# Performance work log

Measured on AMD Instinct MI355X. Metric: run time of the kernel, lower is better.

The kernel has to match this reference:

```python
import jax, jax.numpy as jnp
import numpy as np

N, K, G = 4096, 4096, 128  # out_features, in_features, groupsize


def setup_inputs() -> dict:
    key = jax.random.key(0)
    k1, k2, k3, k4 = jax.random.split(key, 4)
    input = jax.random.normal(k1, (1, 2048, K), dtype=jnp.float32)
    # packed int4 weights: each byte holds two 4-bit codes (high nibble = even k, low = odd k)
    weight_packed = jax.random.randint(k2, (N, K // 2), 0, 256, dtype=jnp.int32)
    scales = jax.random.uniform(k3, (K // G, N), dtype=jnp.float32) * 0.02 + 1e-3
    zeros = jax.random.normal(k4, (K // G, N), dtype=jnp.float32) * 0.05
    scales_and_zeros = jnp.stack([scales, zeros], axis=-1)  # (K//G, N, 2)
    return {"input": input, "weight_packed": weight_packed,
            "scales_and_zeros": scales_and_zeros, "groupsize": G}


def reference(input, weight_packed, scales_and_zeros, groupsize):
    n, k_half = weight_packed.shape
    k = 2 * k_half
    g = k // groupsize
    # unpack two int4 codes per byte: high nibble first (even k index), then low nibble
    hi = (weight_packed >> 4) & 0xF
    lo = weight_packed & 0xF
    q = jnp.stack([hi, lo], axis=-1).reshape(n, k)  # (N, K), codes in [0,15]
    scales = scales_and_zeros[..., 0].T  # (N, G)
    zeros = scales_and_zeros[..., 1].T   # (N, G)
    # group-wise affine dequant: w = (q - 8) * scale + zero
    qg = q.reshape(n, g, groupsize).astype(jnp.float32)
    w = (qg - 8.0) * scales[:, :, None] + zeros[:, :, None]  # (N, G, gs)
    w = w.reshape(n, k)
    # out[..., n] = sum_k input[..., k] * w[n, k]
    return jnp.einsum('bsk,nk->bsn', input, w)
```

## Files before the change

### kernel.cpp

```cpp
#include <hip/hip_runtime.h>
#include <hip/hip_bf16.h>


using bf16x8 = __attribute__((ext_vector_type(8))) short;
using f32x16 = __attribute__((ext_vector_type(16))) float;

#define KK 4096
#define NN 4096
#define NT (KK / 64)

static __device__ __forceinline__ short f2bf(float f) {
    __hip_bfloat16 h = __float2bfloat16(f);
    return __builtin_bit_cast(short, h);
}

#define GLDS16(gptr, lptr) __builtin_amdgcn_global_load_lds( \
    (const __attribute__((address_space(1))) void*)(gptr),   \
    (__attribute__((address_space(3))) void*)(lptr), 16, 0, 0)

#define MFMA32 __builtin_amdgcn_mfma_f32_32x32x16_bf16

__global__ __launch_bounds__(256) void dequant_w(
    const int* __restrict__ W, const float* __restrict__ SZ,
    short* __restrict__ Wd)
{
    const int idx = blockIdx.x * 256 + threadIdx.x;
    const int n   = idx >> 9;
    const int q4  = idx & 511;
    const int kh0 = q4 << 2;
    const int g   = kh0 >> 6;
    const float2 sz = *(const float2*)(SZ + ((size_t)g * NN + n) * 2);
    const float scale = sz.x;
    const float zs    = sz.y - 8.0f * sz.x;
    int4 p = *(const int4*)(W + (size_t)n * (KK / 2) + kh0);
    int vals[4] = {p.x, p.y, p.z, p.w};
    bf16x8 r;
    #pragma unroll
    for (int j = 0; j < 4; ++j) {
        int v = vals[j];
        r[2 * j]     = f2bf((float)((v >> 4) & 0xF) * scale + zs);
        r[2 * j + 1] = f2bf((float)(v & 0xF) * scale + zs);
    }
    *(bf16x8*)&Wd[(size_t)n * KK + (kh0 << 1)] = r;
}

__global__ __launch_bounds__(256) void cvt_a(
    const float* __restrict__ A, short* __restrict__ Ab)
{
    const int idx = blockIdx.x * 256 + threadIdx.x;
    const float4* s = (const float4*)(A + (size_t)idx * 8);
    float4 u = s[0], v = s[1];
    bf16x8 r;
    r[0] = f2bf(u.x); r[1] = f2bf(u.y); r[2] = f2bf(u.z); r[3] = f2bf(u.w);
    r[4] = f2bf(v.x); r[5] = f2bf(v.y); r[6] = f2bf(v.z); r[7] = f2bf(v.w);
    *(bf16x8*)&Ab[(size_t)idx * 8] = r;
}

__global__ __launch_bounds__(512, 2) void gemm_pl(
    const short* __restrict__ Ab, const short* __restrict__ Bb,
    float* __restrict__ C)
{
    __shared__ short sA[3 * 256 * 64];
    __shared__ short sB[3 * 128 * 64];

    const int tid  = threadIdx.x;
    const int lane = tid & 63;
    const int wave = tid >> 6;
    const int wm   = wave >> 1;
    const int wn   = wave & 1;
    const int bm   = blockIdx.y * 256;
    const int bn   = blockIdx.x * 128;

    const int sl = lane >> 3;
    const int sc = (lane & 7) ^ sl;
    const short* aSt = Ab + (size_t)(bm + wave * 32 + sl) * KK + sc * 8;
    const short* bSt = Bb + (size_t)(bn + wave * 16 + sl) * KK + sc * 8;

    const int l31 = lane & 31;
    const int lx  = lane >> 5;
    const int l7  = lane & 7;
    const int px0 = ((0 + lx) ^ l7) * 8;
    const int px1 = ((2 + lx) ^ l7) * 8;
    const int px2 = ((4 + lx) ^ l7) * 8;
    const int px3 = ((6 + lx) ^ l7) * 8;
    const int aRd = (wm * 64 + l31) * 64;
    const int bRd = (wn * 64 + l31) * 64;

    f32x16 acc00 = {}, acc01 = {}, acc10 = {}, acc11 = {};
    bf16x8 pA00, pA01, pA10, pA11, pB00, pB01, pB10, pB11;
    bf16x8 qA00, qA01, qA10, qA11, qB00, qB01, qB10, qB11;

    #pragma unroll
    for (int l = 0; l < 4; ++l)
        GLDS16(aSt + (size_t)l * 8 * KK,      &sA[(wave * 32 + l * 8) * 64]);
    #pragma unroll
    for (int l = 0; l < 2; ++l)
        GLDS16(bSt + (size_t)l * 8 * KK,      &sB[(wave * 16 + l * 8) * 64]);
    #pragma unroll
    for (int l = 0; l < 4; ++l)
        GLDS16(aSt + (size_t)l * 8 * KK + 64, &sA[16384 + (wave * 32 + l * 8) * 64]);
    #pragma unroll
    for (int l = 0; l < 2; ++l)
        GLDS16(bSt + (size_t)l * 8 * KK + 64, &sB[8192 + (wave * 16 + l * 8) * 64]);
    asm volatile("s_waitcnt vmcnt(6)" ::: "memory");
    __builtin_amdgcn_s_barrier();

    pA00 = *(const bf16x8*)&sA[aRd + px0];
    pA01 = *(const bf16x8*)&sA[aRd + px1];
    pA10 = *(const bf16x8*)&sA[aRd + 2048 + px0];
    pA11 = *(const bf16x8*)&sA[aRd + 2048 + px1];
    pB00 = *(const bf16x8*)&sB[bRd + px0];
    pB01 = *(const bf16x8*)&sB[bRd + px1];
    pB10 = *(const bf16x8*)&sB[bRd + 2048 + px0];
    pB11 = *(const bf16x8*)&sB[bRd + 2048 + px1];
    asm volatile("s_waitcnt lgkmcnt(0)" ::: "memory");
    __builtin_amdgcn_sched_barrier(0);

    int cur = 0;
    for (int t = 0; t < NT; ++t) {
        const int nxt1 = (cur == 2) ? 0 : cur + 1;
        const int nxt2 = (nxt1 == 2) ? 0 : nxt1 + 1;
        const short* sAc = &sA[cur * 16384];
        const short* sBc = &sB[cur * 8192];
        const short* sA1 = &sA[nxt1 * 16384];
        const short* sB1 = &sB[nxt1 * 8192];
        short* sAn = &sA[nxt2 * 16384];
        short* sBn = &sB[nxt2 * 8192];
        const bool st = (t + 2 < NT);
        const int gk = (t + 2) * 64;

        qA00 = *(const bf16x8*)&sAc[aRd + px2];
        qA01 = *(const bf16x8*)&sAc[aRd + px3];
        qA10 = *(const bf16x8*)&sAc[aRd + 2048 + px2];
        qA11 = *(const bf16x8*)&sAc[aRd + 2048 + px3];
        qB00 = *(const bf16x8*)&sBc[bRd + px2];
        qB01 = *(const bf16x8*)&sBc[bRd + px3];
        qB10 = *(const bf16x8*)&sBc[bRd + 2048 + px2];
        qB11 = *(const bf16x8*)&sBc[bRd + 2048 + px3];
        if (st) {
            GLDS16(aSt + (size_t)0 * 8 * KK + gk, sAn + (wave * 32 + 0) * 64);
            GLDS16(aSt + (size_t)1 * 8 * KK + gk, sAn + (wave * 32 + 8) * 64);
            GLDS16(bSt + (size_t)0 * 8 * KK + gk, sBn + (wave * 16 + 0) * 64);
        }
        __builtin_amdgcn_sched_barrier(0);

        __builtin_amdgcn_s_setprio(1);
        acc00 = MFMA32(pA00, pB00, acc00, 0, 0, 0);
        acc00 = MFMA32(pA01, pB01, acc00, 0, 0, 0);
        acc01 = MFMA32(pA00, pB10, acc01, 0, 0, 0);
        acc01 = MFMA32(pA01, pB11, acc01, 0, 0, 0);
        acc10 = MFMA32(pA10, pB00, acc10, 0, 0, 0);
        acc10 = MFMA32(pA11, pB01, acc10, 0, 0, 0);
        acc11 = MFMA32(pA10, pB10, acc11, 0, 0, 0);
        acc11 = MFMA32(pA11, pB11, acc11, 0, 0, 0);
        __builtin_amdgcn_s_setprio(0);

        asm volatile("s_waitcnt lgkmcnt(0)" ::: "memory");
        __builtin_amdgcn_sched_barrier(0);
        if (t < NT - 2) {
            asm volatile("s_waitcnt vmcnt(3)" ::: "memory");
        } else {
            asm volatile("s_waitcnt vmcnt(0)" ::: "memory");
        }
        __builtin_amdgcn_s_barrier();

        if (t + 1 < NT) {
            pA00 = *(const bf16x8*)&sA1[aRd + px0];
            pA01 = *(const bf16x8*)&sA1[aRd + px1];
            pA10 = *(const bf16x8*)&sA1[aRd + 2048 + px0];
            pA11 = *(const bf16x8*)&sA1[aRd + 2048 + px1];
            pB00 = *(const bf16x8*)&sB1[bRd + px0];
            pB01 = *(const bf16x8*)&sB1[bRd + px1];
            pB10 = *(const bf16x8*)&sB1[bRd + 2048 + px0];
            pB11 = *(const bf16x8*)&sB1[bRd + 2048 + px1];
        }
        if (st) {
            GLDS16(aSt + (size_t)2 * 8 * KK + gk, sAn + (wave * 32 + 16) * 64);
            GLDS16(aSt + (size_t)3 * 8 * KK + gk, sAn + (wave * 32 + 24) * 64);
            GLDS16(bSt + (size_t)1 * 8 * KK + gk, sBn + (wave * 16 + 8) * 64);
        }
        __builtin_amdgcn_sched_barrier(0);

        __builtin_amdgcn_s_setprio(1);
        acc00 = MFMA32(qA00, qB00, acc00, 0, 0, 0);
        acc00 = MFMA32(qA01, qB01, acc00, 0, 0, 0);
        acc01 = MFMA32(qA00, qB10, acc01, 0, 0, 0);
        acc01 = MFMA32(qA01, qB11, acc01, 0, 0, 0);
        acc10 = MFMA32(qA10, qB00, acc10, 0, 0, 0);
        acc10 = MFMA32(qA11, qB01, acc10, 0, 0, 0);
        acc11 = MFMA32(qA10, qB10, acc11, 0, 0, 0);
        acc11 = MFMA32(qA11, qB11, acc11, 0, 0, 0);
        __builtin_amdgcn_s_setprio(0);

        asm volatile("s_waitcnt lgkmcnt(0)" ::: "memory");
        __builtin_amdgcn_sched_barrier(0);

        cur = nxt1;
    }

    {
        const int crow = lx * 4;
        float* Cp = C + (size_t)(bm + wm * 64) * NN + bn + wn * 64;
        #pragma unroll
        for (int m = 0; m < 2; ++m) {
            #pragma unroll
            for (int qr = 0; qr < 4; ++qr) {
                #pragma unroll
                for (int j = 0; j < 4; ++j) {
                    const int row = m * 32 + crow + j + 8 * qr;
                    float* dst = Cp + (size_t)row * NN + l31;
                    if (m == 0) {
                        dst[0]  = acc00[qr * 4 + j];
                        dst[32] = acc01[qr * 4 + j];
                    } else {
                        dst[0]  = acc10[qr * 4 + j];
                        dst[32] = acc11[qr * 4 + j];
                    }
                }
            }
        }
    }
}

using f32x4 = __attribute__((ext_vector_type(4))) float;
#define LDKF 72
__global__ __launch_bounds__(256) void wq4_gemm_fused(
    const float* __restrict__ A, const int* __restrict__ W,
    const float* __restrict__ SZ, float* __restrict__ C, int M)
{
    __shared__ short sA[128 * LDKF];
    __shared__ short sB[128 * LDKF];
    const int tid = threadIdx.x, lane = tid & 63, wave = tid >> 6;
    const int wr = (wave >> 1) << 6, wc = (wave & 1) << 6;
    const int bm = blockIdx.y * 128, bn = blockIdx.x * 128;
    const int ar = tid >> 2, ac = (tid & 3) << 4;
    const int br = tid >> 1, bh = (tid & 1) << 4;
    const float* Arow0 = A + (size_t)(bm + ar) * KK + ac;
    const float* Arow1 = A + (size_t)(bm + 64 + ar) * KK + ac;
    const int*   Wrow  = W + (size_t)(bn + br) * (KK / 2) + bh;
    const float* SZrow = SZ + (size_t)(bn + br) * 2;
    f32x4 acc[4][4] = {};
    for (int k0 = 0; k0 < KK; k0 += 64) {
        {
            const float4* s0 = (const float4*)(Arow0 + k0);
            const float4* s1 = (const float4*)(Arow1 + k0);
            float4 a0 = s0[0], a1 = s0[1], a2 = s0[2], a3 = s0[3];
            float4 b0 = s1[0], b1 = s1[1], b2 = s1[2], b3 = s1[3];
            auto cvt8 = [](float4 u, float4 v) -> bf16x8 {
                bf16x8 r;
                r[0] = f2bf(u.x); r[1] = f2bf(u.y); r[2] = f2bf(u.z); r[3] = f2bf(u.w);
                r[4] = f2bf(v.x); r[5] = f2bf(v.y); r[6] = f2bf(v.z); r[7] = f2bf(v.w);
                return r;
            };
            *(bf16x8*)&sA[ar * LDKF + ac]            = cvt8(a0, a1);
            *(bf16x8*)&sA[ar * LDKF + ac + 8]        = cvt8(a2, a3);
            *(bf16x8*)&sA[(64 + ar) * LDKF + ac]     = cvt8(b0, b1);
            *(bf16x8*)&sA[(64 + ar) * LDKF + ac + 8] = cvt8(b2, b3);
        }
        {
            const int g = k0 >> 7;
            const float2 sz = *(const float2*)(SZrow + (size_t)g * NN * 2);
            const float scale = sz.x, zs = sz.y - 8.0f * sz.x;
            const int4* src = (const int4*)(Wrow + (k0 >> 1));
            #pragma unroll
            for (int i = 0; i < 4; ++i) {
                int4 p = src[i];
                int vals[4] = {p.x, p.y, p.z, p.w};
                bf16x8 r;
                #pragma unroll
                for (int j = 0; j < 4; ++j) {
                    int v = vals[j];
                    r[2 * j]     = f2bf((float)((v >> 4) & 0xF) * scale + zs);
                    r[2 * j + 1] = f2bf((float)(v & 0xF) * scale + zs);
                }
                *(bf16x8*)&sB[br * LDKF + (bh << 1) + (i << 3)] = r;
            }
        }
        __syncthreads();
        #pragma unroll
        for (int ks = 0; ks < 2; ++ks) {
            const int col = (ks << 5) + ((lane >> 4) << 3);
            bf16x8 af[4], bfr[4];
            #pragma unroll
            for (int m = 0; m < 4; ++m)
                af[m] = *(const bf16x8*)&sA[(wr + m * 16 + (lane & 15)) * LDKF + col];
            #pragma unroll
            for (int n = 0; n < 4; ++n)
                bfr[n] = *(const bf16x8*)&sB[(wc + n * 16 + (lane & 15)) * LDKF + col];
            #pragma unroll
            for (int m = 0; m < 4; ++m)
                #pragma unroll
                for (int n = 0; n < 4; ++n)
                    acc[m][n] = __builtin_amdgcn_mfma_f32_16x16x32_bf16(
                        af[m], bfr[n], acc[m][n], 0, 0, 0);
        }
        __syncthreads();
    }
    float* Cp = C + (size_t)(bm + wr) * NN + bn + wc;
    const int cr = (lane >> 4) << 2, cc = lane & 15;
    #pragma unroll
    for (int m = 0; m < 4; ++m)
        #pragma unroll
        for (int j = 0; j < 4; ++j) {
            float* dst = Cp + (size_t)(m * 16 + cr + j) * NN + cc;
            #pragma unroll
            for (int n = 0; n < 4; ++n) dst[n * 16] = acc[m][n][j];
        }
}

extern "C" void kernel_launch(void* const* d_in, const int* in_sizes, int n_in,
                              void* d_out, int out_size, void* d_ws, size_t ws_size,
                              hipStream_t stream) {
    const float* A  = (const float*)d_in[0];
    const int*   W  = (const int*)d_in[1];
    const float* SZ = (const float*)d_in[2];
    float* C = (float*)d_out;

    const int M = in_sizes[0] / KK;

    const size_t wd_elems = (size_t)NN * KK;
    const size_t ab_elems = (size_t)M * KK;
    const size_t need = (wd_elems + ab_elems) * sizeof(short);

    if (ws_size >= need && (M % 256) == 0) {
        short* Wd = (short*)d_ws;
        short* Ab = Wd + wd_elems;
        dequant_w<<<NN * (KK / 8) / 256, 256, 0, stream>>>(W, SZ, Wd);
        cvt_a<<<(int)(ab_elems / 8 / 256), 256, 0, stream>>>(A, Ab);
        dim3 grid(NN / 128, M / 256);
        gemm_pl<<<grid, dim3(512), 0, stream>>>(Ab, Wd, C);
    } else {
        dim3 grid(NN / 128, M / 128);
        wq4_gemm_fused<<<grid, dim3(256), 0, stream>>>(A, W, SZ, C, M);
    }
}
```

Baseline: 93.78 us.

## Interleave LDS fragment loads with MFMA at finer k-slice granularity

Splits each 64-wide k tile into four 16-wide slices and double-buffers register fragments (even/odd sets) so each slice's LDS reads are issued while the previous slice's MFMAs run. This halves the fragment register footprint and removes the explicit lgkmcnt(0) waits between MFMA groups, relying on compiler-inserted waits. It adds more scheduling barriers and smaller MFMA batches, which could expose LDS latency if the compiler's waits are placed poorly.

```diff
diff --git a/kernel.cpp b/kernel.cpp
--- a/kernel.cpp
+++ b/kernel.cpp
@@ -19,6 +19,7 @@
     (__attribute__((address_space(3))) void*)(lptr), 16, 0, 0)
 
 #define MFMA32 __builtin_amdgcn_mfma_f32_32x32x16_bf16
+#define SBAR() __builtin_amdgcn_sched_barrier(0)
 
 __global__ __launch_bounds__(256) void dequant_w(
     const int* __restrict__ W, const float* __restrict__ SZ,
@@ -87,8 +88,8 @@
     const int bRd = (wn * 64 + l31) * 64;
 
     f32x16 acc00 = {}, acc01 = {}, acc10 = {}, acc11 = {};
-    bf16x8 pA00, pA01, pA10, pA11, pB00, pB01, pB10, pB11;
-    bf16x8 qA00, qA01, qA10, qA11, qB00, qB01, qB10, qB11;
+    bf16x8 eA0, eA1, eB0, eB1;
+    bf16x8 oA0, oA1, oB0, oB1;
 
     #pragma unroll
     for (int l = 0; l < 4; ++l)
@@ -105,16 +106,11 @@
     asm volatile("s_waitcnt vmcnt(6)" ::: "memory");
     __builtin_amdgcn_s_barrier();
 
-    pA00 = *(const bf16x8*)&sA[aRd + px0];
-    pA01 = *(const bf16x8*)&sA[aRd + px1];
-    pA10 = *(const bf16x8*)&sA[aRd + 2048 + px0];
-    pA11 = *(const bf16x8*)&sA[aRd + 2048 + px1];
-    pB00 = *(const bf16x8*)&sB[bRd + px0];
-    pB01 = *(const bf16x8*)&sB[bRd + px1];
-    pB10 = *(const bf16x8*)&sB[bRd + 2048 + px0];
-    pB11 = *(const bf16x8*)&sB[bRd + 2048 + px1];
-    asm volatile("s_waitcnt lgkmcnt(0)" ::: "memory");
-    __builtin_amdgcn_sched_barrier(0);
+    eA0 = *(const bf16x8*)&sA[aRd + px0];
+    eA1 = *(const bf16x8*)&sA[aRd + 2048 + px0];
+    eB0 = *(const bf16x8*)&sB[bRd + px0];
+    eB1 = *(const bf16x8*)&sB[bRd + 2048 + px0];
+    SBAR();
 
     int cur = 0;
     for (int t = 0; t < NT; ++t) {
@@ -129,34 +125,52 @@
         const bool st = (t + 2 < NT);
         const int gk = (t + 2) * 64;
 
-        qA00 = *(const bf16x8*)&sAc[aRd + px2];
-        qA01 = *(const bf16x8*)&sAc[aRd + px3];
-        qA10 = *(const bf16x8*)&sAc[aRd + 2048 + px2];
-        qA11 = *(const bf16x8*)&sAc[aRd + 2048 + px3];
-        qB00 = *(const bf16x8*)&sBc[bRd + px2];
-        qB01 = *(const bf16x8*)&sBc[bRd + px3];
-        qB10 = *(const bf16x8*)&sBc[bRd + 2048 + px2];
-        qB11 = *(const bf16x8*)&sBc[bRd + 2048 + px3];
+        oA0 = *(const bf16x8*)&sAc[aRd + px1];
+        oA1 = *(const bf16x8*)&sAc[aRd + 2048 + px1];
+        oB0 = *(const bf16x8*)&sBc[bRd + px1];
+        oB1 = *(const bf16x8*)&sBc[bRd + 2048 + px1];
+        SBAR();
+        __builtin_amdgcn_s_setprio(1);
+        acc00 = MFMA32(eA0, eB0, acc00, 0, 0, 0);
+        acc01 = MFMA32(eA0, eB1, acc01, 0, 0, 0);
+        acc10 = MFMA32(eA1, eB0, acc10, 0, 0, 0);
+        acc11 = MFMA32(eA1, eB1, acc11, 0, 0, 0);
+        __builtin_amdgcn_s_setprio(0);
+        SBAR();
+
+        eA0 = *(const bf16x8*)&sAc[aRd + px2];
+        eA1 = *(const bf16x8*)&sAc[aRd + 2048 + px2];
+        eB0 = *(const bf16x8*)&sBc[bRd + px2];
+        eB1 = *(const bf16x8*)&sBc[bRd + 2048 + px2];
+        SBAR();
+        __builtin_amdgcn_s_setprio(1);
+        acc00 = MFMA32(oA0, oB0, acc00, 0, 0, 0);
+        acc01 = MFMA32(oA0, oB1, acc01, 0, 0, 0);
+        acc10 = MFMA32(oA1, oB0, acc10, 0, 0, 0);
+        acc11 = MFMA32(oA1, oB1, acc11, 0, 0, 0);
+        __builtin_amdgcn_s_setprio(0);
+        SBAR();
+
+        oA0 = *(const bf16x8*)&sAc[aRd + px3];
+        oA1 = *(const bf16x8*)&sAc[aRd + 2048 + px3];
+        oB0 = *(const bf16x8*)&sBc[bRd + px3];
+        oB1 = *(const bf16x8*)&sBc[bRd + 2048 + px3];
         if (st) {
             GLDS16(aSt + (size_t)0 * 8 * KK + gk, sAn + (wave * 32 + 0) * 64);
             GLDS16(aSt + (size_t)1 * 8 * KK + gk, sAn + (wave * 32 + 8) * 64);
             GLDS16(bSt + (size_t)0 * 8 * KK + gk, sBn + (wave * 16 + 0) * 64);
         }
-        __builtin_amdgcn_sched_barrier(0);
-
+        SBAR();
         __builtin_amdgcn_s_setprio(1);
-        acc00 = MFMA32(pA00, pB00, acc00, 0, 0, 0);
-        acc00 = MFMA32(pA01, pB01, acc00, 0, 0, 0);
-        acc01 = MFMA32(pA00, pB10, acc01, 0, 0, 0);
-        acc01 = MFMA32(pA01, pB11, acc01, 0, 0, 0);
-        acc10 = MFMA32(pA10, pB00, acc10, 0, 0, 0);
-        acc10 = MFMA32(pA11, pB01, acc10, 0, 0, 0);
-        acc11 = MFMA32(pA10, pB10, acc11, 0, 0, 0);
-        acc11 = MFMA32(pA11, pB11, acc11, 0, 0, 0);
+        acc00 = MFMA32(eA0, eB0, acc00, 0, 0, 0);
+        acc01 = MFMA32(eA0, eB1, acc01, 0, 0, 0);
+        acc10 = MFMA32(eA1, eB0, acc10, 0, 0, 0);
+        acc11 = MFMA32(eA1, eB1, acc11, 0, 0, 0);
         __builtin_amdgcn_s_setprio(0);
+        SBAR();
 
         asm volatile("s_waitcnt lgkmcnt(0)" ::: "memory");
-        __builtin_amdgcn_sched_barrier(0);
+        SBAR();
         if (t < NT - 2) {
             asm volatile("s_waitcnt vmcnt(3)" ::: "memory");
         } else {
@@ -165,35 +179,24 @@
         __builtin_amdgcn_s_barrier();
 
         if (t + 1 < NT) {
-            pA00 = *(const bf16x8*)&sA1[aRd + px0];
-            pA01 = *(const bf16x8*)&sA1[aRd + px1];
-            pA10 = *(const bf16x8*)&sA1[aRd + 2048 + px0];
-            pA11 = *(const bf16x8*)&sA1[aRd + 2048 + px1];
-            pB00 = *(const bf16x8*)&sB1[bRd + px0];
-            pB01 = *(const bf16x8*)&sB1[bRd + px1];
-            pB10 = *(const bf16x8*)&sB1[bRd + 2048 + px0];
-            pB11 = *(const bf16x8*)&sB1[bRd + 2048 + px1];
+            eA0 = *(const bf16x8*)&sA1[aRd + px0];
+            eA1 = *(const bf16x8*)&sA1[aRd + 2048 + px0];
+            eB0 = *(const bf16x8*)&sB1[bRd + px0];
+            eB1 = *(const bf16x8*)&sB1[bRd + 2048 + px0];
         }
         if (st) {
             GLDS16(aSt + (size_t)2 * 8 * KK + gk, sAn + (wave * 32 + 16) * 64);
             GLDS16(aSt + (size_t)3 * 8 * KK + gk, sAn + (wave * 32 + 24) * 64);
             GLDS16(bSt + (size_t)1 * 8 * KK + gk, sBn + (wave * 16 + 8) * 64);
         }
-        __builtin_amdgcn_sched_barrier(0);
-
+        SBAR();
         __builtin_amdgcn_s_setprio(1);
-        acc00 = MFMA32(qA00, qB00, acc00, 0, 0, 0);
-        acc00 = MFMA32(qA01, qB01, acc00, 0, 0, 0);
-        acc01 = MFMA32(qA00, qB10, acc01, 0, 0, 0);
-        acc01 = MFMA32(qA01, qB11, acc01, 0, 0, 0);
-        acc10 = MFMA32(qA10, qB00, acc10, 0, 0, 0);
-        acc10 = MFMA32(qA11, qB01, acc10, 0, 0, 0);
-        acc11 = MFMA32(qA10, qB10, acc11, 0, 0, 0);
-        acc11 = MFMA32(qA11, qB11, acc11, 0, 0, 0);
+        acc00 = MFMA32(oA0, oB0, acc00, 0, 0, 0);
+        acc01 = MFMA32(oA0, oB1, acc01, 0, 0, 0);
+        acc10 = MFMA32(oA1, oB0, acc10, 0, 0, 0);
+        acc11 = MFMA32(oA1, oB1, acc11, 0, 0, 0);
         __builtin_amdgcn_s_setprio(0);
-
-        asm volatile("s_waitcnt lgkmcnt(0)" ::: "memory");
-        __builtin_amdgcn_sched_barrier(0);
+        SBAR();
 
         cur = nxt1;
     }
```

Result: slower. 96.23 us (+2.6%).

## Fuse int4 weight dequantization into GEMM mainloop, dropping separate dequant pass

Applied to the files above, without the earlier changes.

Removes the standalone dequant kernel that wrote a full bf16 weight matrix to workspace. The GEMM now loads packed int4 weights and scale/zero pairs into registers, dequantizes them, and writes bf16 tiles to swizzled LDS inside the pipelined loop. All A tile loads move to the first half of each iteration. This removes a large global write and read round trip. In exchange it adds per-block redundant dequant ALU work, register pressure and LDS stores on the MFMA critical path.

```diff
diff --git a/kernel.cpp b/kernel.cpp
--- a/kernel.cpp
+++ b/kernel.cpp
@@ -19,29 +19,17 @@
     (__attribute__((address_space(3))) void*)(lptr), 16, 0, 0)
 
 #define MFMA32 __builtin_amdgcn_mfma_f32_32x32x16_bf16
-
-__global__ __launch_bounds__(256) void dequant_w(
-    const int* __restrict__ W, const float* __restrict__ SZ,
-    short* __restrict__ Wd)
-{
-    const int idx = blockIdx.x * 256 + threadIdx.x;
-    const int n   = idx >> 9;
-    const int q4  = idx & 511;
-    const int kh0 = q4 << 2;
-    const int g   = kh0 >> 6;
-    const float2 sz = *(const float2*)(SZ + ((size_t)g * NN + n) * 2);
-    const float scale = sz.x;
-    const float zs    = sz.y - 8.0f * sz.x;
-    int4 p = *(const int4*)(W + (size_t)n * (KK / 2) + kh0);
-    int vals[4] = {p.x, p.y, p.z, p.w};
+#define SBAR() __builtin_amdgcn_sched_barrier(0)
+
+static __device__ __forceinline__ bf16x8 dq8(int4 p, float s, float zs) {
     bf16x8 r;
+    int v[4] = {p.x, p.y, p.z, p.w};
     #pragma unroll
     for (int j = 0; j < 4; ++j) {
-        int v = vals[j];
-        r[2 * j]     = f2bf((float)((v >> 4) & 0xF) * scale + zs);
-        r[2 * j + 1] = f2bf((float)(v & 0xF) * scale + zs);
-    }
-    *(bf16x8*)&Wd[(size_t)n * KK + (kh0 << 1)] = r;
+        r[2 * j]     = f2bf((float)((v[j] >> 4) & 0xF) * s + zs);
+        r[2 * j + 1] = f2bf((float)(v[j] & 0xF) * s + zs);
+    }
+    return r;
 }
 
 __global__ __launch_bounds__(256) void cvt_a(
@@ -56,9 +44,9 @@
     *(bf16x8*)&Ab[(size_t)idx * 8] = r;
 }
 
-__global__ __launch_bounds__(512, 2) void gemm_pl(
-    const short* __restrict__ Ab, const short* __restrict__ Bb,
-    float* __restrict__ C)
+__global__ __launch_bounds__(512, 2) void gemm_fq(
+    const short* __restrict__ Ab, const int* __restrict__ W,
+    const float* __restrict__ SZ, float* __restrict__ C)
 {
     __shared__ short sA[3 * 256 * 64];
     __shared__ short sB[3 * 128 * 64];
@@ -74,7 +62,13 @@
     const int sl = lane >> 3;
     const int sc = (lane & 7) ^ sl;
     const short* aSt = Ab + (size_t)(bm + wave * 32 + sl) * KK + sc * 8;
-    const short* bSt = Bb + (size_t)(bn + wave * 16 + sl) * KK + sc * 8;
+
+    const int brow = wave * 16 + (lane >> 2);
+    const int bl4  = lane & 3;
+    const int* wSt = W + (size_t)(bn + brow) * (KK / 2) + bl4 * 8;
+    const float* szp = SZ + (size_t)(bn + brow) * 2;
+    const int bw0 = brow * 64 + (((bl4 * 2))     ^ (brow & 7)) * 8;
+    const int bw1 = brow * 64 + (((bl4 * 2) | 1) ^ (brow & 7)) * 8;
 
     const int l31 = lane & 31;
     const int lx  = lane >> 5;
@@ -90,19 +84,26 @@
     bf16x8 pA00, pA01, pA10, pA11, pB00, pB01, pB10, pB11;
     bf16x8 qA00, qA01, qA10, qA11, qB00, qB01, qB10, qB11;
 
+    int4 b00p = *(const int4*)(wSt + 0);
+    int4 b01p = *(const int4*)(wSt + 4);
+    float2 sz0 = *(const float2*)(szp);
+    int4 b10p = *(const int4*)(wSt + 32);
+    int4 b11p = *(const int4*)(wSt + 36);
     #pragma unroll
     for (int l = 0; l < 4; ++l)
         GLDS16(aSt + (size_t)l * 8 * KK,      &sA[(wave * 32 + l * 8) * 64]);
     #pragma unroll
-    for (int l = 0; l < 2; ++l)
-        GLDS16(bSt + (size_t)l * 8 * KK,      &sB[(wave * 16 + l * 8) * 64]);
-    #pragma unroll
     for (int l = 0; l < 4; ++l)
         GLDS16(aSt + (size_t)l * 8 * KK + 64, &sA[16384 + (wave * 32 + l * 8) * 64]);
-    #pragma unroll
-    for (int l = 0; l < 2; ++l)
-        GLDS16(bSt + (size_t)l * 8 * KK + 64, &sB[8192 + (wave * 16 + l * 8) * 64]);
-    asm volatile("s_waitcnt vmcnt(6)" ::: "memory");
+    {
+        const float s = sz0.x, zs = sz0.y - 8.0f * sz0.x;
+        *(bf16x8*)&sB[bw0]        = dq8(b00p, s, zs);
+        *(bf16x8*)&sB[bw1]        = dq8(b01p, s, zs);
+        *(bf16x8*)&sB[8192 + bw0] = dq8(b10p, s, zs);
+        *(bf16x8*)&sB[8192 + bw1] = dq8(b11p, s, zs);
+    }
+    asm volatile("s_waitcnt vmcnt(4)" ::: "memory");
+    asm volatile("s_waitcnt lgkmcnt(0)" ::: "memory");
     __builtin_amdgcn_s_barrier();
 
     pA00 = *(const bf16x8*)&sA[aRd + px0];
@@ -114,7 +115,7 @@
     pB10 = *(const bf16x8*)&sB[bRd + 2048 + px0];
     pB11 = *(const bf16x8*)&sB[bRd + 2048 + px1];
     asm volatile("s_waitcnt lgkmcnt(0)" ::: "memory");
-    __builtin_amdgcn_sched_barrier(0);
+    SBAR();
 
     int cur = 0;
     for (int t = 0; t < NT; ++t) {
@@ -137,12 +138,17 @@
         qB01 = *(const bf16x8*)&sBc[bRd + px3];
         qB10 = *(const bf16x8*)&sBc[bRd + 2048 + px2];
         qB11 = *(const bf16x8*)&sBc[bRd + 2048 + px3];
+        int4 bp0, bp1; float2 szv;
         if (st) {
+            bp0 = *(const int4*)(wSt + (gk >> 1));
+            bp1 = *(const int4*)(wSt + (gk >> 1) + 4);
+            szv = *(const float2*)(szp + (size_t)((t + 2) >> 1) * NN * 2);
             GLDS16(aSt + (size_t)0 * 8 * KK + gk, sAn + (wave * 32 + 0) * 64);
             GLDS16(aSt + (size_t)1 * 8 * KK + gk, sAn + (wave * 32 + 8) * 64);
-            GLDS16(bSt + (size_t)0 * 8 * KK + gk, sBn + (wave * 16 + 0) * 64);
-        }
-        __builtin_amdgcn_sched_barrier(0);
+            GLDS16(aSt + (size_t)2 * 8 * KK + gk, sAn + (wave * 32 + 16) * 64);
+            GLDS16(aSt + (size_t)3 * 8 * KK + gk, sAn + (wave * 32 + 24) * 64);
+        }
+        SBAR();
 
         __builtin_amdgcn_s_setprio(1);
         acc00 = MFMA32(pA00, pB00, acc00, 0, 0, 0);
@@ -155,13 +161,19 @@
         acc11 = MFMA32(pA11, pB11, acc11, 0, 0, 0);
         __builtin_amdgcn_s_setprio(0);
 
-        asm volatile("s_waitcnt lgkmcnt(0)" ::: "memory");
-        __builtin_amdgcn_sched_barrier(0);
-        if (t < NT - 2) {
-            asm volatile("s_waitcnt vmcnt(3)" ::: "memory");
+        if (st) {
+            asm volatile("s_waitcnt vmcnt(4)" ::: "memory");
         } else {
             asm volatile("s_waitcnt vmcnt(0)" ::: "memory");
         }
+        SBAR();
+        if (st) {
+            const float s = szv.x, zs = szv.y - 8.0f * szv.x;
+            *(bf16x8*)&sBn[bw0] = dq8(bp0, s, zs);
+            *(bf16x8*)&sBn[bw1] = dq8(bp1, s, zs);
+        }
+        asm volatile("s_waitcnt lgkmcnt(0)" ::: "memory");
+        SBAR();
         __builtin_amdgcn_s_barrier();
 
         if (t + 1 < NT) {
@@ -174,12 +186,7 @@
             pB10 = *(const bf16x8*)&sB1[bRd + 2048 + px0];
             pB11 = *(const bf16x8*)&sB1[bRd + 2048 + px1];
         }
-        if (st) {
-            GLDS16(aSt + (size_t)2 * 8 * KK + gk, sAn + (wave * 32 + 16) * 64);
-            GLDS16(aSt + (size_t)3 * 8 * KK + gk, sAn + (wave * 32 + 24) * 64);
-            GLDS16(bSt + (size_t)1 * 8 * KK + gk, sBn + (wave * 16 + 8) * 64);
-        }
-        __builtin_amdgcn_sched_barrier(0);
+        SBAR();
 
         __builtin_amdgcn_s_setprio(1);
         acc00 = MFMA32(qA00, qB00, acc00, 0, 0, 0);
@@ -193,7 +200,7 @@
         __builtin_amdgcn_s_setprio(0);
 
         asm volatile("s_waitcnt lgkmcnt(0)" ::: "memory");
-        __builtin_amdgcn_sched_barrier(0);
+        SBAR();
 
         cur = nxt1;
     }
@@ -318,17 +325,14 @@
 
     const int M = in_sizes[0] / KK;
 
-    const size_t wd_elems = (size_t)NN * KK;
     const size_t ab_elems = (size_t)M * KK;
-    const size_t need = (wd_elems + ab_elems) * sizeof(short);
+    const size_t need = ab_elems * sizeof(short);
 
     if (ws_size >= need && (M % 256) == 0) {
-        short* Wd = (short*)d_ws;
-        short* Ab = Wd + wd_elems;
-        dequant_w<<<NN * (KK / 8) / 256, 256, 0, stream>>>(W, SZ, Wd);
+        short* Ab = (short*)d_ws;
         cvt_a<<<(int)(ab_elems / 8 / 256), 256, 0, stream>>>(A, Ab);
         dim3 grid(NN / 128, M / 256);
-        gemm_pl<<<grid, dim3(512), 0, stream>>>(Ab, Wd, C);
+        gemm_fq<<<grid, dim3(512), 0, stream>>>(Ab, W, SZ, C);
     } else {
         dim3 grid(NN / 128, M / 128);
         wq4_gemm_fused<<<grid, dim3(256), 0, stream>>>(A, W, SZ, C, M);
```

Result: slower. 104.0 us (+10.9%).

## Add split-K 256x256-tile GEMM with bf16 partials and reduction kernel

Applied to the files above, without the earlier changes.

Adds a new GEMM path that splits K into two halves across blockIdx.z, using larger 256x256 output tiles per block with double-buffered LDS and eight accumulators per wave. Each half writes bf16 partial results to workspace, and a separate reduce kernel sums them into fp32 output. The aim is better grid occupancy and more MFMA reuse per loaded tile. In exchange it adds extra global traffic for the partials, one more launch, and precision loss from rounding partials to bf16. It also needs a larger workspace and falls back to the old path when that is unavailable.

```diff
diff --git a/kernel.cpp b/kernel.cpp
--- a/kernel.cpp
+++ b/kernel.cpp
@@ -4,21 +4,26 @@
 
 using bf16x8 = __attribute__((ext_vector_type(8))) short;
 using f32x16 = __attribute__((ext_vector_type(16))) float;
+using f32x4  = __attribute__((ext_vector_type(4))) float;
 
 #define KK 4096
 #define NN 4096
-#define NT (KK / 64)
 
 static __device__ __forceinline__ short f2bf(float f) {
     __hip_bfloat16 h = __float2bfloat16(f);
     return __builtin_bit_cast(short, h);
 }
+static __device__ __forceinline__ float bf2f(short u) {
+    unsigned x = ((unsigned)(unsigned short)u) << 16;
+    return __builtin_bit_cast(float, x);
+}
 
 #define GLDS16(gptr, lptr) __builtin_amdgcn_global_load_lds( \
     (const __attribute__((address_space(1))) void*)(gptr),   \
     (__attribute__((address_space(3))) void*)(lptr), 16, 0, 0)
 
 #define MFMA32 __builtin_amdgcn_mfma_f32_32x32x16_bf16
+#define SBAR() __builtin_amdgcn_sched_barrier(0)
 
 __global__ __launch_bounds__(256) void dequant_w(
     const int* __restrict__ W, const float* __restrict__ SZ,
@@ -56,25 +61,26 @@
     *(bf16x8*)&Ab[(size_t)idx * 8] = r;
 }
 
-__global__ __launch_bounds__(512, 2) void gemm_pl(
-    const short* __restrict__ Ab, const short* __restrict__ Bb,
-    float* __restrict__ C)
+__global__ __launch_bounds__(512, 2) void gemm_sk(
+    const short* __restrict__ Ab, const short* __restrict__ Wd,
+    unsigned short* __restrict__ P, int M)
 {
-    __shared__ short sA[3 * 256 * 64];
-    __shared__ short sB[3 * 128 * 64];
+    __shared__ short sA[2 * 256 * 64];
+    __shared__ short sB[2 * 256 * 64];
 
     const int tid  = threadIdx.x;
     const int lane = tid & 63;
     const int wave = tid >> 6;
-    const int wm   = wave >> 1;
-    const int wn   = wave & 1;
+    const int wm   = wave >> 2;
+    const int wn   = wave & 3;
     const int bm   = blockIdx.y * 256;
-    const int bn   = blockIdx.x * 128;
+    const int bn   = blockIdx.x * 256;
+    const size_t kz = (size_t)blockIdx.z * 2048;
 
     const int sl = lane >> 3;
     const int sc = (lane & 7) ^ sl;
-    const short* aSt = Ab + (size_t)(bm + wave * 32 + sl) * KK + sc * 8;
-    const short* bSt = Bb + (size_t)(bn + wave * 16 + sl) * KK + sc * 8;
+    const short* aSt = Ab + (size_t)(bm + wave * 32 + sl) * KK + kz + sc * 8;
+    const short* bSt = Wd + (size_t)(bn + wave * 32 + sl) * KK + kz + sc * 8;
 
     const int l31 = lane & 31;
     const int lx  = lane >> 5;
@@ -83,13 +89,173 @@
     const int px1 = ((2 + lx) ^ l7) * 8;
     const int px2 = ((4 + lx) ^ l7) * 8;
     const int px3 = ((6 + lx) ^ l7) * 8;
-    const int aRd = (wm * 64 + l31) * 64;
+    const int aRd = (wm * 128 + l31) * 64;
     const int bRd = (wn * 64 + l31) * 64;
 
+    f32x16 acc00 = {}, acc01 = {}, acc10 = {}, acc11 = {};
+    f32x16 acc20 = {}, acc21 = {}, acc30 = {}, acc31 = {};
+    bf16x8 eA0, eA1, eA2, eA3, eB0, eB1;
+    bf16x8 oA0, oA1, oA2, oA3, oB0, oB1;
+
+    #pragma unroll
+    for (int l = 0; l < 4; ++l)
+        GLDS16(aSt + (size_t)l * 8 * KK, &sA[(wave * 32 + l * 8) * 64]);
+    #pragma unroll
+    for (int l = 0; l < 4; ++l)
+        GLDS16(bSt + (size_t)l * 8 * KK, &sB[(wave * 32 + l * 8) * 64]);
+    asm volatile("s_waitcnt vmcnt(0)" ::: "memory");
+    __builtin_amdgcn_s_barrier();
+
+    eA0 = *(const bf16x8*)&sA[aRd + px0];
+    eA1 = *(const bf16x8*)&sA[aRd + 2048 + px0];
+    eA2 = *(const bf16x8*)&sA[aRd + 4096 + px0];
+    eA3 = *(const bf16x8*)&sA[aRd + 6144 + px0];
+    eB0 = *(const bf16x8*)&sB[bRd + px0];
+    eB1 = *(const bf16x8*)&sB[bRd + 2048 + px0];
+    asm volatile("s_waitcnt lgkmcnt(0)" ::: "memory");
+    SBAR();
+
+#define MM8(XA0, XA1, XA2, XA3, XB0, XB1)            \
+    __builtin_amdgcn_s_setprio(1);                   \
+    acc00 = MFMA32(XA0, XB0, acc00, 0, 0, 0);        \
+    acc01 = MFMA32(XA0, XB1, acc01, 0, 0, 0);        \
+    acc10 = MFMA32(XA1, XB0, acc10, 0, 0, 0);        \
+    acc11 = MFMA32(XA1, XB1, acc11, 0, 0, 0);        \
+    acc20 = MFMA32(XA2, XB0, acc20, 0, 0, 0);        \
+    acc21 = MFMA32(XA2, XB1, acc21, 0, 0, 0);        \
+    acc30 = MFMA32(XA3, XB0, acc30, 0, 0, 0);        \
+    acc31 = MFMA32(XA3, XB1, acc31, 0, 0, 0);        \
+    __builtin_amdgcn_s_setprio(0);
+
+    for (int t = 0; t < 32; ++t) {
+        const int cur = t & 1;
+        const short* sAc = &sA[cur * 16384];
+        const short* sBc = &sB[cur * 16384];
+        short* sAn = &sA[(cur ^ 1) * 16384];
+        short* sBn = &sB[(cur ^ 1) * 16384];
+        const bool st = (t + 1 < 32);
+        const size_t gk = (size_t)(t + 1) * 64;
+
+        oA0 = *(const bf16x8*)&sAc[aRd + px1];
+        oA1 = *(const bf16x8*)&sAc[aRd + 2048 + px1];
+        oA2 = *(const bf16x8*)&sAc[aRd + 4096 + px1];
+        oA3 = *(const bf16x8*)&sAc[aRd + 6144 + px1];
+        oB0 = *(const bf16x8*)&sBc[bRd + px1];
+        oB1 = *(const bf16x8*)&sBc[bRd + 2048 + px1];
+        if (st) {
+            GLDS16(aSt + (size_t)0 * 8 * KK + gk, sAn + (wave * 32 + 0) * 64);
+            GLDS16(aSt + (size_t)1 * 8 * KK + gk, sAn + (wave * 32 + 8) * 64);
+            GLDS16(aSt + (size_t)2 * 8 * KK + gk, sAn + (wave * 32 + 16) * 64);
+            GLDS16(aSt + (size_t)3 * 8 * KK + gk, sAn + (wave * 32 + 24) * 64);
+        }
+        SBAR();
+        MM8(eA0, eA1, eA2, eA3, eB0, eB1)
+        SBAR();
+
+        eA0 = *(const bf16x8*)&sAc[aRd + px2];
+        eA1 = *(const bf16x8*)&sAc[aRd + 2048 + px2];
+        eA2 = *(const bf16x8*)&sAc[aRd + 4096 + px2];
+        eA3 = *(const bf16x8*)&sAc[aRd + 6144 + px2];
+        eB0 = *(const bf16x8*)&sBc[bRd + px2];
+        eB1 = *(const bf16x8*)&sBc[bRd + 2048 + px2];
+        if (st) {
+            GLDS16(bSt + (size_t)0 * 8 * KK + gk, sBn + (wave * 32 + 0) * 64);
+            GLDS16(bSt + (size_t)1 * 8 * KK + gk, sBn + (wave * 32 + 8) * 64);
+            GLDS16(bSt + (size_t)2 * 8 * KK + gk, sBn + (wave * 32 + 16) * 64);
+            GLDS16(bSt + (size_t)3 * 8 * KK + gk, sBn + (wave * 32 + 24) * 64);
+        }
+        SBAR();
+        MM8(oA0, oA1, oA2, oA3, oB0, oB1)
+        SBAR();
+
+        oA0 = *(const bf16x8*)&sAc[aRd + px3];
+        oA1 = *(const bf16x8*)&sAc[aRd + 2048 + px3];
+        oA2 = *(const bf16x8*)&sAc[aRd + 4096 + px3];
+        oA3 = *(const bf16x8*)&sAc[aRd + 6144 + px3];
+        oB0 = *(const bf16x8*)&sBc[bRd + px3];
+        oB1 = *(const bf16x8*)&sBc[bRd + 2048 + px3];
+        SBAR();
+        MM8(eA0, eA1, eA2, eA3, eB0, eB1)
+        asm volatile("s_waitcnt lgkmcnt(0)" ::: "memory");
+        SBAR();
+        asm volatile("s_waitcnt vmcnt(0)" ::: "memory");
+        __builtin_amdgcn_s_barrier();
+
+        if (st) {
+            eA0 = *(const bf16x8*)&sAn[aRd + px0];
+            eA1 = *(const bf16x8*)&sAn[aRd + 2048 + px0];
+            eA2 = *(const bf16x8*)&sAn[aRd + 4096 + px0];
+            eA3 = *(const bf16x8*)&sAn[aRd + 6144 + px0];
+            eB0 = *(const bf16x8*)&sBn[bRd + px0];
+            eB1 = *(const bf16x8*)&sBn[bRd + 2048 + px0];
+        }
+        SBAR();
+        MM8(oA0, oA1, oA2, oA3, oB0, oB1)
+        asm volatile("s_waitcnt lgkmcnt(0)" ::: "memory");
+        SBAR();
+    }
+#undef MM8
+
+    {
+        const int crow = lx * 4;
+        unsigned short* Pp = P + (size_t)blockIdx.z * ((size_t)M * NN);
+#define EPI(F, AC0, AC1)                                                     \
+        { _Pragma("unroll")                                                  \
+          for (int qr = 0; qr < 4; ++qr) {                                   \
+            _Pragma("unroll")                                                \
+            for (int j = 0; j < 4; ++j) {                                    \
+                const int row = bm + wm * 128 + (F) * 32 + crow + j + 8 * qr;\
+                unsigned short* d = Pp + (size_t)row * NN + bn + wn * 64 + l31;\
+                d[0]  = (unsigned short)f2bf(AC0[qr * 4 + j]);               \
+                d[32] = (unsigned short)f2bf(AC1[qr * 4 + j]);               \
+            } } }
+        EPI(0, acc00, acc01)
+        EPI(1, acc10, acc11)
+        EPI(2, acc20, acc21)
+        EPI(3, acc30, acc31)
+#undef EPI
+    }
+}
+
+__global__ __launch_bounds__(256) void reduce_k(
+    const unsigned short* __restrict__ P, float* __restrict__ C, int MN)
+{
+    const int idx = blockIdx.x * 256 + threadIdx.x;
+    const bf16x8 a = *(const bf16x8*)(P + (size_t)idx * 8);
+    const bf16x8 b = *(const bf16x8*)(P + (size_t)MN + (size_t)idx * 8);
+    float4 o0, o1;
+    o0.x = bf2f(a[0]) + bf2f(b[0]);
+    o0.y = bf2f(a[1]) + bf2f(b[1]);
+    o0.z = bf2f(a[2]) + bf2f(b[2]);
+    o0.w = bf2f(a[3]) + bf2f(b[3]);
+    o1.x = bf2f(a[4]) + bf2f(b[4]);
+    o1.y = bf2f(a[5]) + bf2f(b[5]);
+    o1.z = bf2f(a[6]) + bf2f(b[6]);
+    o1.w = bf2f(a[7]) + bf2f(b[7]);
+    float* Cp = C + (size_t)idx * 8;
+    *(float4*)Cp = o0;
+    *(float4*)(Cp + 4) = o1;
+}
+
+__global__ __launch_bounds__(512, 2) void gemm_pl(
+    const short* __restrict__ Ab, const short* __restrict__ Bb,
+    float* __restrict__ C)
+{
+    __shared__ short sA[3 * 256 * 64];
+    __shared__ short sB[3 * 128 * 64];
+    const int tid = threadIdx.x, lane = tid & 63, wave = tid >> 6;
+    const int wm = wave >> 1, wn = wave & 1;
+    const int bm = blockIdx.y * 256, bn = blockIdx.x * 128;
+    const int sl = lane >> 3, sc = (lane & 7) ^ sl;
+    const short* aSt = Ab + (size_t)(bm + wave * 32 + sl) * KK + sc * 8;
+    const short* bSt = Bb + (size_t)(bn + wave * 16 + sl) * KK + sc * 8;
+    const int l31 = lane & 31, lx = lane >> 5, l7 = lane & 7;
+    const int px0 = ((0 + lx) ^ l7) * 8, px1 = ((2 + lx) ^ l7) * 8;
+    const int px2 = ((4 + lx) ^ l7) * 8, px3 = ((6 + lx) ^ l7) * 8;
+    const int aRd = (wm * 64 + l31) * 64, bRd = (wn * 64 + l31) * 64;
     f32x16 acc00 = {}, acc01 = {}, acc10 = {}, acc11 = {};
     bf16x8 pA00, pA01, pA10, pA11, pB00, pB01, pB10, pB11;
     bf16x8 qA00, qA01, qA10, qA11, qB00, qB01, qB10, qB11;
-
     #pragma unroll
     for (int l = 0; l < 4; ++l)
         GLDS16(aSt + (size_t)l * 8 * KK,      &sA[(wave * 32 + l * 8) * 64]);
@@ -104,7 +270,6 @@
         GLDS16(bSt + (size_t)l * 8 * KK + 64, &sB[8192 + (wave * 16 + l * 8) * 64]);
     asm volatile("s_waitcnt vmcnt(6)" ::: "memory");
     __builtin_amdgcn_s_barrier();
-
     pA00 = *(const bf16x8*)&sA[aRd + px0];
     pA01 = *(const bf16x8*)&sA[aRd + px1];
     pA10 = *(const bf16x8*)&sA[aRd + 2048 + px0];
@@ -114,10 +279,9 @@
     pB10 = *(const bf16x8*)&sB[bRd + 2048 + px0];
     pB11 = *(const bf16x8*)&sB[bRd + 2048 + px1];
     asm volatile("s_waitcnt lgkmcnt(0)" ::: "memory");
-    __builtin_amdgcn_sched_barrier(0);
-
+    SBAR();
     int cur = 0;
-    for (int t = 0; t < NT; ++t) {
+    for (int t = 0; t < 64; ++t) {
         const int nxt1 = (cur == 2) ? 0 : cur + 1;
         const int nxt2 = (nxt1 == 2) ? 0 : nxt1 + 1;
         const short* sAc = &sA[cur * 16384];
@@ -126,9 +290,8 @@
         const short* sB1 = &sB[nxt1 * 8192];
         short* sAn = &sA[nxt2 * 16384];
         short* sBn = &sB[nxt2 * 8192];
-        const bool st = (t + 2 < NT);
+        const bool st = (t + 2 < 64);
         const int gk = (t + 2) * 64;
-
         qA00 = *(const bf16x8*)&sAc[aRd + px2];
         qA01 = *(const bf16x8*)&sAc[aRd + px3];
         qA10 = *(const bf16x8*)&sAc[aRd + 2048 + px2];
@@ -142,8 +305,7 @@
             GLDS16(aSt + (size_t)1 * 8 * KK + gk, sAn + (wave * 32 + 8) * 64);
             GLDS16(bSt + (size_t)0 * 8 * KK + gk, sBn + (wave * 16 + 0) * 64);
         }
-        __builtin_amdgcn_sched_barrier(0);
-
+        SBAR();
         __builtin_amdgcn_s_setprio(1);
         acc00 = MFMA32(pA00, pB00, acc00, 0, 0, 0);
         acc00 = MFMA32(pA01, pB01, acc00, 0, 0, 0);
@@ -154,17 +316,15 @@
         acc11 = MFMA32(pA10, pB10, acc11, 0, 0, 0);
         acc11 = MFMA32(pA11, pB11, acc11, 0, 0, 0);
         __builtin_amdgcn_s_setprio(0);
-
         asm volatile("s_waitcnt lgkmcnt(0)" ::: "memory");
-        __builtin_amdgcn_sched_barrier(0);
-        if (t < NT - 2) {
+        SBAR();
+        if (t < 62) {
             asm volatile("s_waitcnt vmcnt(3)" ::: "memory");
         } else {
             asm volatile("s_waitcnt vmcnt(0)" ::: "memory");
         }
         __builtin_amdgcn_s_barrier();
-
-        if (t + 1 < NT) {
+        if (t + 1 < 64) {
             pA00 = *(const bf16x8*)&sA1[aRd + px0];
             pA01 = *(const bf16x8*)&sA1[aRd + px1];
             pA10 = *(const bf16x8*)&sA1[aRd + 2048 + px0];
@@ -179,8 +339,7 @@
             GLDS16(aSt + (size_t)3 * 8 * KK + gk, sAn + (wave * 32 + 24) * 64);
             GLDS16(bSt + (size_t)1 * 8 * KK + gk, sBn + (wave * 16 + 8) * 64);
         }
-        __builtin_amdgcn_sched_barrier(0);
-
+        SBAR();
         __builtin_amdgcn_s_setprio(1);
         acc00 = MFMA32(qA00, qB00, acc00, 0, 0, 0);
         acc00 = MFMA32(qA01, qB01, acc00, 0, 0, 0);
@@ -191,13 +350,10 @@
         acc11 = MFMA32(qA10, qB10, acc11, 0, 0, 0);
         acc11 = MFMA32(qA11, qB11, acc11, 0, 0, 0);
         __builtin_amdgcn_s_setprio(0);
-
         asm volatile("s_waitcnt lgkmcnt(0)" ::: "memory");
-        __builtin_amdgcn_sched_barrier(0);
-
+        SBAR();
         cur = nxt1;
     }
-
     {
         const int crow = lx * 4;
         float* Cp = C + (size_t)(bm + wm * 64) * NN + bn + wn * 64;
@@ -222,7 +378,6 @@
     }
 }
 
-using f32x4 = __attribute__((ext_vector_type(4))) float;
 #define LDKF 72
 __global__ __launch_bounds__(256) void wq4_gemm_fused(
     const float* __restrict__ A, const int* __restrict__ W,
@@ -318,15 +473,27 @@
 
     const int M = in_sizes[0] / KK;
 
-    const size_t wd_elems = (size_t)NN * KK;
-    const size_t ab_elems = (size_t)M * KK;
-    const size_t need = (wd_elems + ab_elems) * sizeof(short);
-
-    if (ws_size >= need && (M % 256) == 0) {
+    const size_t wd_e = (size_t)NN * KK;
+    const size_t ab_e = (size_t)M * KK;
+    const size_t p_e  = 2 * (size_t)M * NN;
+    const size_t need_sk = (wd_e + ab_e + p_e) * sizeof(short);
+    const size_t need_r5 = (wd_e + ab_e) * sizeof(short);
+
+    if (ws_size >= need_sk && (M % 256) == 0) {
         short* Wd = (short*)d_ws;
-        short* Ab = Wd + wd_elems;
+        short* Ab = Wd + wd_e;
+        unsigned short* P = (unsigned short*)(Ab + ab_e);
         dequant_w<<<NN * (KK / 8) / 256, 256, 0, stream>>>(W, SZ, Wd);
-        cvt_a<<<(int)(ab_elems / 8 / 256), 256, 0, stream>>>(A, Ab);
+        cvt_a<<<(int)(ab_e / 8 / 256), 256, 0, stream>>>(A, Ab);
+        dim3 grid(NN / 256, M / 256, 2);
+        gemm_sk<<<grid, dim3(512), 0, stream>>>(Ab, Wd, P, M);
+        const int MN = M * NN;
+        reduce_k<<<MN / 8 / 256, 256, 0, stream>>>(P, C, MN);
+    } else if (ws_size >= need_r5 && (M % 256) == 0) {
+        short* Wd = (short*)d_ws;
+        short* Ab = Wd + wd_e;
+        dequant_w<<<NN * (KK / 8) / 256, 256, 0, stream>>>(W, SZ, Wd);
+        cvt_a<<<(int)(ab_e / 8 / 256), 256, 0, stream>>>(A, Ab);
         dim3 grid(NN / 128, M / 256);
         gemm_pl<<<grid, dim3(512), 0, stream>>>(Ab, Wd, C);
     } else {
```

Measured after the change: 101.3 us. 1.08x slower.
